# Optimization experiments

Hardware: AMD Instinct MI355X
Metric: run time of the kernel (lower is better)

## Reference

```python
import jax, jax.numpy as jnp
import numpy as np

B, Hs, Ws, C = 1, 48, 48, 768
NH = 12
HD = C // NH          # 64
L = Hs * Ws           # 2304
THETA = 10000.0
SCALE = HD ** -0.5
EPS = 1e-5

# relative coord index table: rel_idx[i, j] = i - j + (H - 1), as in _setup_rel_pos
_REL_IDX = jnp.asarray(np.arange(Hs)[:, None] - np.arange(Ws)[None, :] + (Hs - 1))


def _rope_cos_sin():
    """2D axial RoPE angles (compute_axial_cis): [L, HD//2] cos/sin tables."""
    nf = HD // 4
    freqs = 1.0 / (THETA ** (np.arange(0, HD, 4)[:nf].astype(np.float32) / HD))
    t = np.arange(L, dtype=np.float32)
    tx = t % Hs               # x coord cycles fastest (init_t_xy)
    ty = np.floor(t / Hs)
    ang = np.concatenate([np.outer(tx, freqs), np.outer(ty, freqs)], axis=-1)  # [L, HD//2]
    return jnp.asarray(np.cos(ang)), jnp.asarray(np.sin(ang))


def _layernorm(x, w, b):
    mu = x.mean(-1, keepdims=True)
    var = ((x - mu) ** 2).mean(-1, keepdims=True)
    return (x - mu) * jax.lax.rsqrt(var + EPS) * w + b


def _apply_rope(t, cos, sin):
    # t: [B, NH, L, HD]; view as complex pairs (even=real, odd=imag)
    tr = t.reshape(*t.shape[:-1], HD // 2, 2)
    re, im = tr[..., 0], tr[..., 1]
    out = jnp.stack([re * cos - im * sin, re * sin + im * cos], axis=-1)
    return out.reshape(t.shape)


def setup_inputs() -> dict:
    key = jax.random.key(0)
    ks = jax.random.split(key, 8)
    def rn(k, shape, std=0.02):
        return jax.random.normal(k, shape, dtype=jnp.float32) * std
    return {
        "x": jax.random.normal(ks[0], (B, Hs, Ws, C), dtype=jnp.float32),
        "ln1_w": jnp.ones((C,), jnp.float32),
        "ln1_b": jnp.zeros((C,), jnp.float32),
        "qkv_w": rn(ks[1], (3 * C, C)),
        "qkv_b": jnp.zeros((3 * C,), jnp.float32),
        "rel_pos_h": rn(ks[2], (2 * Hs - 1, HD)),
        "rel_pos_w": rn(ks[3], (2 * Ws - 1, HD)),
        "proj_w": rn(ks[4], (C, C)),
        "proj_b": jnp.zeros((C,), jnp.float32),
        "ln2_w": jnp.ones((C,), jnp.float32),
        "ln2_b": jnp.zeros((C,), jnp.float32),
        "fc1_w": rn(ks[5], (4 * C, C)),
        "fc1_b": jnp.zeros((4 * C,), jnp.float32),
        "fc2_w": rn(ks[6], (C, 4 * C)),
        "fc2_b": jnp.zeros((C,), jnp.float32),
    }


def reference(x, ln1_w, ln1_b, qkv_w, qkv_b, rel_pos_h, rel_pos_w, proj_w, proj_b,
              ln2_w, ln2_b, fc1_w, fc1_b, fc2_w, fc2_b):
    shortcut = x
    h = _layernorm(x, ln1_w, ln1_b)                         # [B,H,W,C]
    qkv = h.reshape(B, L, C) @ qkv_w.T + qkv_b              # [B,L,3C]
    qkv = qkv.reshape(B, L, 3, NH, HD).transpose(2, 0, 3, 1, 4)
    q, k, v = qkv[0], qkv[1], qkv[2]                        # [B,NH,L,HD]

    cos, sin = _rope_cos_sin()
    cos, sin = cos[None, None], sin[None, None]
    q = _apply_rope(q, cos, sin)
    k = _apply_rope(k, cos, sin)

    # Decomposed relative-position bias; math-equivalent to concat_rel_pos
    # (q' = [q*rescale, gathered-rel-vecs], k' = [k, one-hots]) followed by SDPA.
    rq = q.reshape(B, NH, Hs, Ws, HD)
    Rh = rel_pos_h[_REL_IDX]                                # [Hs, Hs(kh), HD]
    Rw = rel_pos_w[_REL_IDX]                                # [Ws, Ws(kw), HD]
    bias_h = jnp.einsum('bnhwc,hkc->bnhwk', rq, Rh)         # over key-row
    bias_w = jnp.einsum('bnhwc,wkc->bnhwk', rq, Rw)         # over key-col

    scores = jnp.einsum('bnqc,bnkc->bnqk', q, k) * SCALE    # [B,NH,L,L]
    scores = scores.reshape(B, NH, Hs, Ws, Hs, Ws) + bias_h[..., :, None] + bias_w[..., None, :]
    attn = jax.nn.softmax(scores.reshape(B, NH, L, L), axis=-1)
    out = jnp.einsum('bnqk,bnkc->bnqc', attn, v)            # [B,NH,L,HD]
    out = out.transpose(0, 2, 1, 3).reshape(B, L, C) @ proj_w.T + proj_b

    x = shortcut + out.reshape(B, Hs, Ws, C)
    h = _layernorm(x, ln2_w, ln2_b)
    h = jax.nn.gelu(h @ fc1_w.T + fc1_b, approximate=False)
    x = x + (h @ fc2_w.T + fc2_b)
    return x
```

## Files before the change

### kernel.cpp

```cpp
#include <hip/hip_runtime.h>
#include <math.h>

#define LTOK 2304
#define CDIM 768
#define NHEAD 12
#define HDIM 64
#define HS 48

typedef short s16x8 __attribute__((ext_vector_type(8)));
typedef float f32x4 __attribute__((ext_vector_type(4)));

__device__ __forceinline__ unsigned short f2b(float f) {
  __bf16 b = (__bf16)f;
  return __builtin_bit_cast(unsigned short, b);
}
__device__ __forceinline__ float b2f(unsigned short u) {
  unsigned int x = ((unsigned int)u) << 16;
  return __builtin_bit_cast(float, x);
}

__device__ __forceinline__ void gld_lds16(void* lds, const void* g) {
  __builtin_amdgcn_global_load_lds(
      (const __attribute__((address_space(1))) unsigned int*)g,
      (__attribute__((address_space(3))) unsigned int*)lds, 16, 0, 0);
}

__global__ __launch_bounds__(256) void f2b4_kernel(const float* __restrict__ a0,
                                                   const float* __restrict__ a1,
                                                   const float* __restrict__ a2,
                                                   const float* __restrict__ a3,
                                                   unsigned short* __restrict__ d0,
                                                   unsigned short* __restrict__ d1,
                                                   unsigned short* __restrict__ d2,
                                                   unsigned short* __restrict__ d3) {
  const int v = blockIdx.x * 256 + threadIdx.x;
  const float* src;
  unsigned short* dst;
  int off;
  if (v < 221184)      { src = a0; dst = d0; off = v; }
  else if (v < 294912) { src = a1; dst = d1; off = v - 221184; }
  else if (v < 589824) { src = a2; dst = d2; off = v - 294912; }
  else                 { src = a3; dst = d3; off = v - 589824; }
  const int i = off * 8;
  float4 v0 = *(const float4*)(src + i);
  float4 v1 = *(const float4*)(src + i + 4);
  alignas(16) unsigned short o[8] = {f2b(v0.x), f2b(v0.y), f2b(v0.z), f2b(v0.w),
                                     f2b(v1.x), f2b(v1.y), f2b(v1.z), f2b(v1.w)};
  *(uint4*)(dst + i) = *(const uint4*)o;
}

__global__ __launch_bounds__(256) void ln_kernel(const float* __restrict__ x,
                                                 const float* __restrict__ w,
                                                 const float* __restrict__ b,
                                                 unsigned short* __restrict__ out) {
  const int row = blockIdx.x;
  const int t = threadIdx.x;
  const float* xr = x + (size_t)row * CDIM;
  float v0 = xr[t], v1 = xr[t + 256], v2 = xr[t + 512];
  float s = v0 + v1 + v2;
  float ss = v0 * v0 + v1 * v1 + v2 * v2;
#pragma unroll
  for (int off = 32; off > 0; off >>= 1) {
    s += __shfl_down(s, off, 64);
    ss += __shfl_down(ss, off, 64);
  }
  __shared__ float rs[4], rss[4];
  if ((t & 63) == 0) { rs[t >> 6] = s; rss[t >> 6] = ss; }
  __syncthreads();
  float S = rs[0] + rs[1] + rs[2] + rs[3];
  float SS = rss[0] + rss[1] + rss[2] + rss[3];
  const float inv_c = 1.0f / (float)CDIM;
  float mu = S * inv_c;
  float var = SS * inv_c - mu * mu;
  float inv = rsqrtf(var + 1e-5f);
  unsigned short* orow = out + (size_t)row * CDIM;
  orow[t]       = f2b((v0 - mu) * inv * w[t]       + b[t]);
  orow[t + 256] = f2b((v1 - mu) * inv * w[t + 256] + b[t + 256]);
  orow[t + 512] = f2b((v2 - mu) * inv * w[t + 512] + b[t + 512]);
}

template <bool GELU, bool RES, bool OUTBF>
__global__ __launch_bounds__(256) void mfma_gemm(const unsigned short* __restrict__ A,
                                                 const unsigned short* __restrict__ B,
                                                 const float* __restrict__ bias,
                                                 const float* __restrict__ res,
                                                 void* __restrict__ Cout,
                                                 int M, int N, int K) {
  __shared__ unsigned short As[128 * 32];
  __shared__ unsigned short Bs[128 * 32];
  const int t = threadIdx.x;
  const int lane = t & 63;
  const int w = t >> 6;
  const int wm = w >> 1, wn = w & 1;
  const int bm = blockIdx.y * 128, bn = blockIdx.x * 128;

  f32x4 acc[4][4] = {};

  const int c0 = 2 * w, c1 = 2 * w + 1;
  const int srow = lane >> 2;
  const int skof = (lane & 3) * 8;
  const unsigned short* Abase = A + (size_t)bm * K + skof;
  const unsigned short* Bbase = B + (size_t)bn * K + skof;
  const int lr = lane & 15, lk = (lane >> 4) * 8, lg = lane >> 4;

  for (int k0 = 0; k0 < K; k0 += 32) {
    gld_lds16(As + c0 * 512, Abase + (size_t)(c0 * 16 + srow) * K + k0);
    gld_lds16(As + c1 * 512, Abase + (size_t)(c1 * 16 + srow) * K + k0);
    gld_lds16(Bs + c0 * 512, Bbase + (size_t)(c0 * 16 + srow) * K + k0);
    gld_lds16(Bs + c1 * 512, Bbase + (size_t)(c1 * 16 + srow) * K + k0);
    __syncthreads();
    s16x8 a[4], b[4];
#pragma unroll
    for (int m = 0; m < 4; ++m)
      a[m] = *(const s16x8*)&As[(wm * 64 + m * 16 + lr) * 32 + lk];
#pragma unroll
    for (int n = 0; n < 4; ++n)
      b[n] = *(const s16x8*)&Bs[(wn * 64 + n * 16 + lr) * 32 + lk];
#pragma unroll
    for (int m = 0; m < 4; ++m)
#pragma unroll
      for (int n = 0; n < 4; ++n)
        acc[m][n] = __builtin_amdgcn_mfma_f32_16x16x32_bf16(a[m], b[n], acc[m][n], 0, 0, 0);
    __syncthreads();
  }

#pragma unroll
  for (int n = 0; n < 4; ++n) {
    const int col = bn + wn * 64 + n * 16 + lr;
    const float bc = bias[col];
#pragma unroll
    for (int m = 0; m < 4; ++m) {
#pragma unroll
      for (int j = 0; j < 4; ++j) {
        const int row = bm + wm * 64 + m * 16 + lg * 4 + j;
        float v = acc[m][n][j] + bc;
        if (GELU) v = 0.5f * v * (1.0f + erff(v * 0.70710678118654752f));
        if (RES) v += res[(size_t)row * N + col];
        if (OUTBF) ((unsigned short*)Cout)[(size_t)row * N + col] = f2b(v);
        else       ((float*)Cout)[(size_t)row * N + col] = v;
      }
    }
  }
}

template <bool GELU, bool RES, bool OUTBF>
__global__ __launch_bounds__(256) void gemm64(const unsigned short* __restrict__ A,
                                              const unsigned short* __restrict__ B,
                                              const float* __restrict__ bias,
                                              const float* __restrict__ res,
                                              void* __restrict__ Cout,
                                              int M, int N, int K) {
  __shared__ unsigned short As[64 * 32];
  __shared__ unsigned short Bs[128 * 32];
  const int t = threadIdx.x;
  const int lane = t & 63;
  const int w = t >> 6;
  const int wm = w >> 1, wn = w & 1;
  const int bm = blockIdx.y * 64, bn = blockIdx.x * 128;

  f32x4 acc[2][4] = {};

  const int srow = lane >> 2;
  const int skof = (lane & 3) * 8;
  const unsigned short* Abase = A + (size_t)bm * K + skof;
  const unsigned short* Bbase = B + (size_t)bn * K + skof;
  const int lr = lane & 15, lk = (lane >> 4) * 8, lg = lane >> 4;

  for (int k0 = 0; k0 < K; k0 += 32) {
    gld_lds16(As + w * 512, Abase + (size_t)(w * 16 + srow) * K + k0);
    gld_lds16(Bs + w * 512, Bbase + (size_t)(w * 16 + srow) * K + k0);
    gld_lds16(Bs + (4 + w) * 512, Bbase + (size_t)((4 + w) * 16 + srow) * K + k0);
    __syncthreads();
    s16x8 a[2], b[4];
#pragma unroll
    for (int m = 0; m < 2; ++m)
      a[m] = *(const s16x8*)&As[(wm * 32 + m * 16 + lr) * 32 + lk];
#pragma unroll
    for (int n = 0; n < 4; ++n)
      b[n] = *(const s16x8*)&Bs[(wn * 64 + n * 16 + lr) * 32 + lk];
#pragma unroll
    for (int m = 0; m < 2; ++m)
#pragma unroll
      for (int n = 0; n < 4; ++n)
        acc[m][n] = __builtin_amdgcn_mfma_f32_16x16x32_bf16(a[m], b[n], acc[m][n], 0, 0, 0);
    __syncthreads();
  }

#pragma unroll
  for (int n = 0; n < 4; ++n) {
    const int col = bn + wn * 64 + n * 16 + lr;
    const float bc = bias[col];
#pragma unroll
    for (int m = 0; m < 2; ++m) {
#pragma unroll
      for (int j = 0; j < 4; ++j) {
        const int row = bm + wm * 32 + m * 16 + lg * 4 + j;
        float v = acc[m][n][j] + bc;
        if (GELU) v = 0.5f * v * (1.0f + erff(v * 0.70710678118654752f));
        if (RES) v += res[(size_t)row * N + col];
        if (OUTBF) ((unsigned short*)Cout)[(size_t)row * N + col] = f2b(v);
        else       ((float*)Cout)[(size_t)row * N + col] = v;
      }
    }
  }
}

__global__ __launch_bounds__(256) void rope_cs_kernel(float* __restrict__ cs,
                                                      float* __restrict__ sn) {
  const int idx = blockIdx.x * 256 + threadIdx.x;
  const int l = idx >> 5;
  const int i = idx & 31;
  const int j = i & 15;
  const float f = __expf(-(float)j * 0.57564627324851142f);
  const float coord = (i < 16) ? (float)(l % HS) : (float)(l / HS);
  const float ang = coord * f;
  cs[idx] = cosf(ang);
  sn[idx] = sinf(ang);
}

__global__ __launch_bounds__(256) void prep_kernel(const float* __restrict__ qkv,
                                                   const float* __restrict__ cs,
                                                   const float* __restrict__ sn,
                                                   unsigned short* __restrict__ Qb,
                                                   unsigned short* __restrict__ Kb,
                                                   unsigned short* __restrict__ Vb) {
  __shared__ unsigned short Vs[64 * 72];
  const int t = threadIdx.x;
  const int l0 = blockIdx.x * 64, n = blockIdx.y;
  const int r = t >> 2, c = t & 3;
  const int l = l0 + r;
  const float* base = qkv + (size_t)l * (3 * CDIM) + n * HDIM + c * 16;
#pragma unroll
  for (int pq = 0; pq < 2; ++pq) {
    const float* src = base + pq * CDIM;
    const float qs = pq ? 1.0f : 0.125f;
    alignas(16) unsigned short o[16];
#pragma unroll
    for (int i = 0; i < 4; ++i) {
      float4 v = *(const float4*)(src + i * 4);
      const int pr = c * 8 + i * 2;
      const float c0 = cs[l * 32 + pr],     s0 = sn[l * 32 + pr];
      const float c1 = cs[l * 32 + pr + 1], s1 = sn[l * 32 + pr + 1];
      o[i * 4 + 0] = f2b((v.x * c0 - v.y * s0) * qs);
      o[i * 4 + 1] = f2b((v.x * s0 + v.y * c0) * qs);
      o[i * 4 + 2] = f2b((v.z * c1 - v.w * s1) * qs);
      o[i * 4 + 3] = f2b((v.z * s1 + v.w * c1) * qs);
    }
    unsigned short* dst = (pq ? Kb : Qb) + ((size_t)n * LTOK + l) * HDIM + c * 16;
    *(uint4*)dst = *(const uint4*)o;
    *(uint4*)(dst + 8) = *(const uint4*)(o + 8);
  }
  {
    const float* vsrc = base + 2 * CDIM;
    alignas(16) unsigned short vo[16];
#pragma unroll
    for (int i = 0; i < 4; ++i) {
      float4 v = *(const float4*)(vsrc + i * 4);
      vo[i * 4 + 0] = f2b(v.x); vo[i * 4 + 1] = f2b(v.y);
      vo[i * 4 + 2] = f2b(v.z); vo[i * 4 + 3] = f2b(v.w);
    }
    *(uint4*)&Vs[r * 72 + c * 16] = *(const uint4*)vo;
    *(uint4*)&Vs[r * 72 + c * 16 + 8] = *(const uint4*)(vo + 8);
  }
  __syncthreads();
  {
    const int d = t >> 2, kc16 = (t & 3) * 16;
    alignas(16) unsigned short o[16];
#pragma unroll
    for (int i = 0; i < 16; ++i) o[i] = Vs[(kc16 + i) * 72 + d];
    const int kb = (l0 + kc16) >> 3;
    unsigned short* dst0 = Vb + ((size_t)(n * (LTOK / 8) + kb) * 64 + d) * 8;
    unsigned short* dst1 = Vb + ((size_t)(n * (LTOK / 8) + kb + 1) * 64 + d) * 8;
    *(uint4*)dst0 = *(const uint4*)o;
    *(uint4*)dst1 = *(const uint4*)(o + 8);
  }
}

__global__ __launch_bounds__(256) void attn_mfma(const unsigned short* __restrict__ Qb,
                                                 const unsigned short* __restrict__ Kb,
                                                 const unsigned short* __restrict__ Vb,
                                                 const float* __restrict__ relh,
                                                 const float* __restrict__ relw,
                                                 unsigned short* __restrict__ out) {
  __shared__ __align__(16) unsigned char smem[74752];
  unsigned short* const K_lds = (unsigned short*)(smem);
  unsigned short* const V_lds = (unsigned short*)(smem + 24576);
  unsigned short* const P_lds = (unsigned short*)(smem + 53248);
  float* const bh_t = (float*)(smem + 62464);
  unsigned short* const Q_s = (unsigned short*)(smem + 53248);

  const int t = threadIdx.x;
  const int lane = t & 63, w = t >> 6;
  const int p = lane & 15, g = lane >> 4;
  const int l0 = blockIdx.x * 64, n = blockIdx.y;

  const unsigned short* Khead = Kb + (size_t)n * LTOK * HDIM;
  const unsigned short* Vhead = Vb + (size_t)n * (LTOK / 8) * 64 * 8;

  {
    const int r = t >> 2, c = t & 3;
    const unsigned short* src = Qb + ((size_t)n * LTOK + l0 + r) * HDIM + c * 16;
    uint4 v0 = *(const uint4*)src;
    uint4 v1 = *(const uint4*)(src + 8);
    *(uint4*)&Q_s[r * 72 + c * 16] = v0;
    *(uint4*)&Q_s[r * 72 + c * 16 + 8] = v1;
  }
  __syncthreads();

  const int rowb = lane >> 3;
  const int srcc = (lane & 7) ^ rowb;
  const int kc0 = w, kc1 = w + 4, kc2 = w + 8;

  {
    gld_lds16(K_lds + kc0 * 512, Khead + (size_t)(kc0 * 8 + rowb) * HDIM + srcc * 8);
    gld_lds16(K_lds + kc1 * 512, Khead + (size_t)(kc1 * 8 + rowb) * HDIM + srcc * 8);
    gld_lds16(K_lds + kc2 * 512, Khead + (size_t)(kc2 * 8 + rowb) * HDIM + srcc * 8);
    gld_lds16(V_lds + kc0 * 512, Vhead + kc0 * 512 + lane * 8);
    gld_lds16(V_lds + kc1 * 512, Vhead + kc1 * 512 + lane * 8);
    gld_lds16(V_lds + kc2 * 512, Vhead + kc2 * 512 + lane * 8);
  }
  if (t < 128) *(uint4*)&V_lds[6144 + t * 8] = uint4{0u, 0u, 0u, 0u};
  else         *(uint4*)&V_lds[7168 + 6144 + (t - 128) * 8] = uint4{0u, 0u, 0u, 0u};

  const s16x8 qf0 = *(const s16x8*)&Q_s[(w * 16 + p) * 72 + g * 8];
  const s16x8 qf1 = *(const s16x8*)&Q_s[(w * 16 + p) * 72 + 32 + g * 8];

  const int qh_lane = (l0 + lane) / 48;
#pragma unroll
  for (int i = 0; i < 12; ++i) {
    const int kh = w + 4 * i;
    const float* rrow = relh + (size_t)(qh_lane - kh + 47) * HDIM;
    float acc = 0.f;
#pragma unroll
    for (int c8 = 0; c8 < 8; ++c8) {
      s16x8 qv = *(const s16x8*)&Q_s[lane * 72 + c8 * 8];
      float4 ra = *(const float4*)&rrow[c8 * 8];
      float4 rb = *(const float4*)&rrow[c8 * 8 + 4];
      acc += b2f((unsigned short)qv[0]) * ra.x + b2f((unsigned short)qv[1]) * ra.y +
             b2f((unsigned short)qv[2]) * ra.z + b2f((unsigned short)qv[3]) * ra.w +
             b2f((unsigned short)qv[4]) * rb.x + b2f((unsigned short)qv[5]) * rb.y +
             b2f((unsigned short)qv[6]) * rb.z + b2f((unsigned short)qv[7]) * rb.w;
    }
    bh_t[kh * 64 + lane] = acc * 8.0f;
  }

  float bwreg[12];
  {
    const int qrow = w * 16 + p;
    const int qw_lane = (l0 + qrow) % 48;
#pragma unroll
    for (int mb = 0; mb < 3; ++mb)
#pragma unroll
      for (int jj = 0; jj < 4; ++jj) {
        const int j = 16 * mb + 4 * g + jj;
        const float* rrow = relw + (size_t)(qw_lane - j + 47) * HDIM;
        float acc = 0.f;
#pragma unroll
        for (int c8 = 0; c8 < 8; ++c8) {
          s16x8 qv = *(const s16x8*)&Q_s[qrow * 72 + c8 * 8];
          float4 ra = *(const float4*)&rrow[c8 * 8];
          float4 rb = *(const float4*)&rrow[c8 * 8 + 4];
          acc += b2f((unsigned short)qv[0]) * ra.x + b2f((unsigned short)qv[1]) * ra.y +
                 b2f((unsigned short)qv[2]) * ra.z + b2f((unsigned short)qv[3]) * ra.w +
                 b2f((unsigned short)qv[4]) * rb.x + b2f((unsigned short)qv[5]) * rb.y +
                 b2f((unsigned short)qv[6]) * rb.z + b2f((unsigned short)qv[7]) * rb.w;
        }
        bwreg[mb * 4 + jj] = acc * 8.0f;
      }
  }
  __syncthreads();

  {
    uint2 z = {0u, 0u};
    *(uint2*)&P_lds[(w * 16 + p) * 72 + 48 + 4 * g] = z;
  }

  float lsum = 0.f;
  f32x4 accO[4] = {};
  const int sw0 = g ^ (p & 7);
  const int sw1 = (g + 4) ^ (p & 7);
  unsigned short* const Pw = P_lds + w * 16 * 72;

#pragma unroll 1
  for (int kt = 0; kt < 24; ++kt) {
    const int ko = (kt & 1) * 6144;
    const int vo = (kt & 1) * 7168;
    if (kt < 23) {
      const int nko = 6144 - ko, nvo = 7168 - vo;
      const int kb = (kt + 1) * 96;
      const int vb = (kt + 1) * 12;
      gld_lds16(K_lds + nko + kc0 * 512, Khead + (size_t)(kb + kc0 * 8 + rowb) * HDIM + srcc * 8);
      gld_lds16(K_lds + nko + kc1 * 512, Khead + (size_t)(kb + kc1 * 8 + rowb) * HDIM + srcc * 8);
      gld_lds16(K_lds + nko + kc2 * 512, Khead + (size_t)(kb + kc2 * 8 + rowb) * HDIM + srcc * 8);
      gld_lds16(V_lds + nvo + kc0 * 512, Vhead + (vb + kc0) * 512 + lane * 8);
      gld_lds16(V_lds + nvo + kc1 * 512, Vhead + (vb + kc1) * 512 + lane * 8);
      gld_lds16(V_lds + nvo + kc2 * 512, Vhead + (vb + kc2) * 512 + lane * 8);
    }

#pragma unroll 1
    for (int h = 0; h < 2; ++h) {
      f32x4 st[3] = {};
      __builtin_amdgcn_s_setprio(1);
#pragma unroll
      for (int mb = 0; mb < 3; ++mb) {
        const int krow = ko + (h * 48 + 16 * mb + p) * 64;
        s16x8 kf0 = *(const s16x8*)&K_lds[krow + sw0 * 8];
        s16x8 kf1 = *(const s16x8*)&K_lds[krow + sw1 * 8];
        st[mb] = __builtin_amdgcn_mfma_f32_16x16x32_bf16(kf0, qf0, st[mb], 0, 0, 0);
        st[mb] = __builtin_amdgcn_mfma_f32_16x16x32_bf16(kf1, qf1, st[mb], 0, 0, 0);
      }
      __builtin_amdgcn_s_setprio(0);

      const float bhv = bh_t[(2 * kt + h) * 64 + w * 16 + p] - 8.0f;
      float pv[12], ps = 0.f;
#pragma unroll
      for (int mb = 0; mb < 3; ++mb)
#pragma unroll
        for (int jj = 0; jj < 4; ++jj) {
          const float sv = st[mb][jj] + bhv + bwreg[mb * 4 + jj];
          pv[mb * 4 + jj] = __expf(sv);
          ps += pv[mb * 4 + jj];
        }
      lsum += ps;

#pragma unroll
      for (int mb = 0; mb < 3; ++mb) {
        unsigned int lo = (unsigned int)f2b(pv[mb * 4 + 0]) | ((unsigned int)f2b(pv[mb * 4 + 1]) << 16);
        unsigned int hi = (unsigned int)f2b(pv[mb * 4 + 2]) | ((unsigned int)f2b(pv[mb * 4 + 3]) << 16);
        uint2 val = {lo, hi};
        *(uint2*)&Pw[p * 72 + 16 * mb + 4 * g] = val;
      }

      const s16x8 pf0 = *(const s16x8*)&Pw[p * 72 + g * 8];
      const s16x8 pf1 = *(const s16x8*)&Pw[p * 72 + 32 + g * 8];
      __builtin_amdgcn_s_setprio(1);
#pragma unroll
      for (int db = 0; db < 4; ++db) {
        const int drow = 16 * db + p;
        s16x8 vf0 = *(const s16x8*)&V_lds[vo + ((6 * h + g) * 64 + drow) * 8];
        s16x8 vf1 = *(const s16x8*)&V_lds[vo + ((6 * h + 4 + g) * 64 + drow) * 8];
        accO[db] = __builtin_amdgcn_mfma_f32_16x16x32_bf16(vf0, pf0, accO[db], 0, 0, 0);
        accO[db] = __builtin_amdgcn_mfma_f32_16x16x32_bf16(vf1, pf1, accO[db], 0, 0, 0);
      }
      __builtin_amdgcn_s_setprio(0);
    }

    __syncthreads();
  }

  float ls = lsum + __shfl_xor(lsum, 16, 64);
  ls += __shfl_xor(ls, 32, 64);
  const float inv = 1.0f / ls;
  unsigned short* orow = out + (size_t)(l0 + w * 16 + p) * CDIM + n * HDIM;
#pragma unroll
  for (int db = 0; db < 4; ++db) {
    unsigned int lo = (unsigned int)f2b(accO[db][0] * inv) | ((unsigned int)f2b(accO[db][1] * inv) << 16);
    unsigned int hi = (unsigned int)f2b(accO[db][2] * inv) | ((unsigned int)f2b(accO[db][3] * inv) << 16);
    uint2 val = {lo, hi};
    *(uint2*)&orow[16 * db + 4 * g] = val;
  }
}

extern "C" void kernel_launch(void* const* d_in, const int* in_sizes, int n_in,
                              void* d_out, int out_size, void* d_ws, size_t ws_size,
                              hipStream_t stream) {
  const float* x     = (const float*)d_in[0];
  const float* ln1w  = (const float*)d_in[1];
  const float* ln1b  = (const float*)d_in[2];
  const float* qkvw  = (const float*)d_in[3];
  const float* qkvb  = (const float*)d_in[4];
  const float* relh  = (const float*)d_in[5];
  const float* relw  = (const float*)d_in[6];
  const float* projw = (const float*)d_in[7];
  const float* projb = (const float*)d_in[8];
  const float* ln2w  = (const float*)d_in[9];
  const float* ln2b  = (const float*)d_in[10];
  const float* fc1w  = (const float*)d_in[11];
  const float* fc1b  = (const float*)d_in[12];
  const float* fc2w  = (const float*)d_in[13];
  const float* fc2b  = (const float*)d_in[14];
  float* out = (float*)d_out;
  float* ws = (float*)d_ws;

  float* qkv = ws;
  float* x1  = qkv + (size_t)LTOK * 3 * CDIM;
  float* cs  = x1 + (size_t)LTOK * CDIM;
  float* sn  = cs + (size_t)LTOK * 32;
  unsigned short* h_bf    = (unsigned short*)(sn + (size_t)LTOK * 32);
  unsigned short* attn_bf = h_bf + (size_t)LTOK * CDIM;
  unsigned short* wq      = attn_bf + (size_t)LTOK * CDIM;
  unsigned short* wproj   = wq + (size_t)3 * CDIM * CDIM;
  unsigned short* wfc1    = wproj + (size_t)CDIM * CDIM;
  unsigned short* wfc2    = wfc1 + (size_t)4 * CDIM * CDIM;
  unsigned short* Qb      = (unsigned short*)x1;
  unsigned short* Kb      = Qb + (size_t)NHEAD * LTOK * HDIM;
  unsigned short* Vb      = wq;
  unsigned short* m1_bf   = (unsigned short*)qkv;

  f2b4_kernel<<<3456, 256, 0, stream>>>(qkvw, projw, fc1w, fc2w, wq, wproj, wfc1, wfc2);

  ln_kernel<<<LTOK, 256, 0, stream>>>(x, ln1w, ln1b, h_bf);
  mfma_gemm<false, false, false><<<dim3(18, 18), 256, 0, stream>>>(
      h_bf, wq, qkvb, nullptr, qkv, LTOK, 3 * CDIM, CDIM);
  rope_cs_kernel<<<288, 256, 0, stream>>>(cs, sn);
  prep_kernel<<<dim3(36, 12), 256, 0, stream>>>(qkv, cs, sn, Qb, Kb, Vb);
  attn_mfma<<<dim3(36, 12), 256, 0, stream>>>(Qb, Kb, Vb, relh, relw, attn_bf);
  gemm64<false, true, false><<<dim3(6, 36), 256, 0, stream>>>(
      attn_bf, wproj, projb, x, x1, LTOK, CDIM, CDIM);
  ln_kernel<<<LTOK, 256, 0, stream>>>(x1, ln2w, ln2b, h_bf);
  mfma_gemm<true, false, true><<<dim3(24, 18), 256, 0, stream>>>(
      h_bf, wfc1, fc1b, nullptr, m1_bf, LTOK, 4 * CDIM, CDIM);
  gemm64<false, true, false><<<dim3(6, 36), 256, 0, stream>>>(
      m1_bf, wfc2, fc2b, x1, out, LTOK, CDIM, 4 * CDIM);
}
```

Baseline: 242.1 us.

## Double-buffer LDS tiles in MFMA GEMMs and raise wave priority around MFMAs

Both bf16 GEMM kernels now hold two LDS buffers per operand. The next K-slice is loaded with global_load_lds while the current slice is consumed, replacing the load, sync, compute, sync pattern with a single barrier per iteration. s_setprio is raised around the MFMA block so compute-phase waves get scheduling priority. This doubles LDS use per block, which may lower occupancy. Correctness relies on the single __syncthreads ordering the async LDS writes before the next read.

```diff
diff --git a/kernel.cpp b/kernel.cpp
--- a/kernel.cpp
+++ b/kernel.cpp
@@ -86,8 +86,8 @@
                                                  const float* __restrict__ res,
                                                  void* __restrict__ Cout,
                                                  int M, int N, int K) {
-  __shared__ unsigned short As[128 * 32];
-  __shared__ unsigned short Bs[128 * 32];
+  __shared__ unsigned short As[2 * 4096];
+  __shared__ unsigned short Bs[2 * 4096];
   const int t = threadIdx.x;
   const int lane = t & 63;
   const int w = t >> 6;
@@ -102,25 +102,39 @@
   const unsigned short* Abase = A + (size_t)bm * K + skof;
   const unsigned short* Bbase = B + (size_t)bn * K + skof;
   const int lr = lane & 15, lk = (lane >> 4) * 8, lg = lane >> 4;
-
-  for (int k0 = 0; k0 < K; k0 += 32) {
-    gld_lds16(As + c0 * 512, Abase + (size_t)(c0 * 16 + srow) * K + k0);
-    gld_lds16(As + c1 * 512, Abase + (size_t)(c1 * 16 + srow) * K + k0);
-    gld_lds16(Bs + c0 * 512, Bbase + (size_t)(c0 * 16 + srow) * K + k0);
-    gld_lds16(Bs + c1 * 512, Bbase + (size_t)(c1 * 16 + srow) * K + k0);
-    __syncthreads();
+  const int nk = K >> 5;
+
+  gld_lds16(As + c0 * 512, Abase + (size_t)(c0 * 16 + srow) * K);
+  gld_lds16(As + c1 * 512, Abase + (size_t)(c1 * 16 + srow) * K);
+  gld_lds16(Bs + c0 * 512, Bbase + (size_t)(c0 * 16 + srow) * K);
+  gld_lds16(Bs + c1 * 512, Bbase + (size_t)(c1 * 16 + srow) * K);
+  __syncthreads();
+
+#pragma unroll 1
+  for (int ks = 0; ks < nk; ++ks) {
+    const int off = (ks & 1) * 4096;
+    if (ks + 1 < nk) {
+      const int noff = 4096 - off;
+      const int k1 = (ks + 1) * 32;
+      gld_lds16(As + noff + c0 * 512, Abase + (size_t)(c0 * 16 + srow) * K + k1);
+      gld_lds16(As + noff + c1 * 512, Abase + (size_t)(c1 * 16 + srow) * K + k1);
+      gld_lds16(Bs + noff + c0 * 512, Bbase + (size_t)(c0 * 16 + srow) * K + k1);
+      gld_lds16(Bs + noff + c1 * 512, Bbase + (size_t)(c1 * 16 + srow) * K + k1);
+    }
     s16x8 a[4], b[4];
 #pragma unroll
     for (int m = 0; m < 4; ++m)
-      a[m] = *(const s16x8*)&As[(wm * 64 + m * 16 + lr) * 32 + lk];
+      a[m] = *(const s16x8*)&As[off + (wm * 64 + m * 16 + lr) * 32 + lk];
 #pragma unroll
     for (int n = 0; n < 4; ++n)
-      b[n] = *(const s16x8*)&Bs[(wn * 64 + n * 16 + lr) * 32 + lk];
+      b[n] = *(const s16x8*)&Bs[off + (wn * 64 + n * 16 + lr) * 32 + lk];
+    __builtin_amdgcn_s_setprio(1);
 #pragma unroll
     for (int m = 0; m < 4; ++m)
 #pragma unroll
       for (int n = 0; n < 4; ++n)
         acc[m][n] = __builtin_amdgcn_mfma_f32_16x16x32_bf16(a[m], b[n], acc[m][n], 0, 0, 0);
+    __builtin_amdgcn_s_setprio(0);
     __syncthreads();
   }
 
@@ -150,8 +164,8 @@
                                               const float* __restrict__ res,
                                               void* __restrict__ Cout,
                                               int M, int N, int K) {
-  __shared__ unsigned short As[64 * 32];
-  __shared__ unsigned short Bs[128 * 32];
+  __shared__ unsigned short As[2 * 2048];
+  __shared__ unsigned short Bs[2 * 4096];
   const int t = threadIdx.x;
   const int lane = t & 63;
   const int w = t >> 6;
@@ -165,24 +179,38 @@
   const unsigned short* Abase = A + (size_t)bm * K + skof;
   const unsigned short* Bbase = B + (size_t)bn * K + skof;
   const int lr = lane & 15, lk = (lane >> 4) * 8, lg = lane >> 4;
-
-  for (int k0 = 0; k0 < K; k0 += 32) {
-    gld_lds16(As + w * 512, Abase + (size_t)(w * 16 + srow) * K + k0);
-    gld_lds16(Bs + w * 512, Bbase + (size_t)(w * 16 + srow) * K + k0);
-    gld_lds16(Bs + (4 + w) * 512, Bbase + (size_t)((4 + w) * 16 + srow) * K + k0);
-    __syncthreads();
+  const int nk = K >> 5;
+
+  gld_lds16(As + w * 512, Abase + (size_t)(w * 16 + srow) * K);
+  gld_lds16(Bs + w * 512, Bbase + (size_t)(w * 16 + srow) * K);
+  gld_lds16(Bs + (4 + w) * 512, Bbase + (size_t)((4 + w) * 16 + srow) * K);
+  __syncthreads();
+
+#pragma unroll 1
+  for (int ks = 0; ks < nk; ++ks) {
+    const int offA = (ks & 1) * 2048;
+    const int offB = (ks & 1) * 4096;
+    if (ks + 1 < nk) {
+      const int nA = 2048 - offA, nB = 4096 - offB;
+      const int k1 = (ks + 1) * 32;
+      gld_lds16(As + nA + w * 512, Abase + (size_t)(w * 16 + srow) * K + k1);
+      gld_lds16(Bs + nB + w * 512, Bbase + (size_t)(w * 16 + srow) * K + k1);
+      gld_lds16(Bs + nB + (4 + w) * 512, Bbase + (size_t)((4 + w) * 16 + srow) * K + k1);
+    }
     s16x8 a[2], b[4];
 #pragma unroll
     for (int m = 0; m < 2; ++m)
-      a[m] = *(const s16x8*)&As[(wm * 32 + m * 16 + lr) * 32 + lk];
+      a[m] = *(const s16x8*)&As[offA + (wm * 32 + m * 16 + lr) * 32 + lk];
 #pragma unroll
     for (int n = 0; n < 4; ++n)
-      b[n] = *(const s16x8*)&Bs[(wn * 64 + n * 16 + lr) * 32 + lk];
+      b[n] = *(const s16x8*)&Bs[offB + (wn * 64 + n * 16 + lr) * 32 + lk];
+    __builtin_amdgcn_s_setprio(1);
 #pragma unroll
     for (int m = 0; m < 2; ++m)
 #pragma unroll
       for (int n = 0; n < 4; ++n)
         acc[m][n] = __builtin_amdgcn_mfma_f32_16x16x32_bf16(a[m], b[n], acc[m][n], 0, 0, 0);
+    __builtin_amdgcn_s_setprio(0);
     __syncthreads();
   }
 
```

Result: faster. 235.9 us (-2.5%).
